# Kernel optimization log

Measured on AMD Instinct MI355X. Metric: run time of the kernel, lower is better.

## Reference

```python
import jax, jax.numpy as jnp
import numpy as np

S, B, IN = 8, 8192, 2      # obs seq_len, batch, input_size
E, H, OUT, PRED = 256, 1024, 2, 12  # embed, rnn_size, output_size, pred_len


def setup_inputs() -> dict:
    key = jax.random.key(0)
    ks = jax.random.split(key, 20)
    w = lambda k, shape, fan: (jax.random.normal(k, shape, jnp.float32) / np.sqrt(fan))
    return {
        "obs_traj": jax.random.normal(ks[0], (S, B, IN), jnp.float32),
        # input embedding Linear(IN -> E)
        "W_emb": w(ks[1], (E, IN), IN), "b_emb": jnp.zeros((E,), jnp.float32),
        # LSTM layer 0: input E -> H  (torch gate order i,f,g,o)
        "W_ih0": w(ks[2], (4 * H, E), E), "W_hh0": w(ks[3], (4 * H, H), H),
        "b_ih0": jnp.zeros((4 * H,), jnp.float32), "b_hh0": jnp.zeros((4 * H,), jnp.float32),
        # LSTM layer 1: input H -> H
        "W_ih1": w(ks[4], (4 * H, H), H), "W_hh1": w(ks[5], (4 * H, H), H),
        "b_ih1": jnp.zeros((4 * H,), jnp.float32), "b_hh1": jnp.zeros((4 * H,), jnp.float32),
        # output_seq MLP: H -> 32 -> 16 -> OUT
        "W1": w(ks[6], (32, H), H), "b1": jnp.zeros((32,), jnp.float32),
        "W2": w(ks[7], (16, 32), 32), "b2": jnp.zeros((16,), jnp.float32),
        "W3": w(ks[8], (OUT, 16), 16), "b3": jnp.zeros((OUT,), jnp.float32),
    }


def reference(obs_traj, W_emb, b_emb, W_ih0, W_hh0, b_ih0, b_hh0,
              W_ih1, W_hh1, b_ih1, b_hh1, W1, b1, W2, b2, W3, b3):
    # Dropout layers are identity in eval mode.
    def embed(x):
        return jax.nn.relu(x @ W_emb.T + b_emb)

    def cell(x, h, c, Wih, Whh, bih, bhh):
        g = x @ Wih.T + h @ Whh.T + (bih + bhh)          # [B, 4H]
        i, f, gg, o = jnp.split(g, 4, axis=-1)
        c = jax.nn.sigmoid(f) * c + jax.nn.sigmoid(i) * jnp.tanh(gg)
        h = jax.nn.sigmoid(o) * jnp.tanh(c)
        return h, c

    def lstm_step(hc, x):
        h0, c0, h1, c1 = hc
        h0, c0 = cell(x, h0, c0, W_ih0, W_hh0, b_ih0, b_hh0)
        h1, c1 = cell(h0, h1, c1, W_ih1, W_hh1, b_ih1, b_hh1)
        return (h0, c0, h1, c1), h1

    def mlp(h):
        h = jax.nn.relu(h @ W1.T + b1)
        h = jax.nn.relu(h @ W2.T + b2)
        return h @ W3.T + b3

    z = jnp.zeros((B, H), obs_traj.dtype)
    hc = (z, z, z, z)

    # --- encoding: run LSTM over the observed trajectory ---
    emb_obs = embed(obs_traj)                             # [S, B, E]
    hc, _ = jax.lax.scan(lambda c, x: lstm_step(c, x), hc, emb_obs)

    curr = obs_traj[-1]                                   # [B, IN]
    curr_emb = embed(curr)

    def dec_step(carry, _):
        hc, curr, curr_emb = carry
        hc, out = lstm_step(hc, curr_emb)                 # out: [B, H]
        nxt = curr + mlp(out)                             # displacement decode
        return (hc, nxt, embed(nxt)), nxt

    _, preds = jax.lax.scan(dec_step, (hc, curr, curr_emb), None, length=PRED)
    return preds                                          # [PRED, B, OUT]
```

## Files before the change

### kernel.cpp

```cpp
#include <hip/hip_runtime.h>
#include <hip/hip_bf16.h>
#include <stdint.h>

typedef __hip_bfloat16 bf16;
typedef __attribute__((ext_vector_type(8))) short bf16x8;
typedef __attribute__((ext_vector_type(4))) float f32x4;
typedef __attribute__((ext_vector_type(8))) unsigned short us8;

#define NB 8192
#define NE 256
#define NH 1024

__device__ __forceinline__ float bf2f(unsigned short u) {
  union { unsigned int i; float f; } x; x.i = ((unsigned int)u) << 16; return x.f;
}
__device__ __forceinline__ float sigm(float x) {
  return __builtin_amdgcn_rcpf(1.f + __expf(-x));
}
__device__ __forceinline__ float tanh_f(float x) {
  return 1.f - 2.f * __builtin_amdgcn_rcpf(1.f + __expf(2.f * x));
}

#define BAR() __builtin_amdgcn_s_barrier()
#define LGKM0() do { asm volatile("s_waitcnt lgkmcnt(0)" ::: "memory"); \
                     __builtin_amdgcn_sched_barrier(0); } while (0)
#define VMW(N) asm volatile("s_waitcnt vmcnt(" #N ")" ::: "memory")

#define MFMA32(MH)                                                            \
  do {                                                                        \
    __builtin_amdgcn_s_setprio(1);                                            \
    _Pragma("unroll") for (int i_ = 0; i_ < 4; ++i_)                          \
      _Pragma("unroll") for (int g_ = 0; g_ < 4; ++g_) {                      \
        acc[(MH)*4 + i_][g_] = __builtin_amdgcn_mfma_f32_16x16x32_bf16(       \
            af[i_], bv[g_], acc[(MH)*4 + i_][g_], 0, 0, 0);                   \
        acc[(MH)*4 + i_][g_] = __builtin_amdgcn_mfma_f32_16x16x32_bf16(       \
            af[4 + i_], bv[4 + g_], acc[(MH)*4 + i_][g_], 0, 0, 0);           \
      }                                                                       \
    __builtin_amdgcn_s_setprio(0);                                            \
  } while (0)

#define LDA8(BUF, MH)                                                         \
  do {                                                                        \
    const char* Ab_ = (const char*)&As[BUF][0][0];                            \
    _Pragma("unroll") for (int i_ = 0; i_ < 4; ++i_) {                        \
      int ro_ = (wr * 128 + (MH)*64 + i_ * 16 + l15) * 128;                   \
      af[i_]     = *(const bf16x8*)(Ab_ + ro_ + co0);                         \
      af[4 + i_] = *(const bf16x8*)(Ab_ + ro_ + co1);                         \
    }                                                                         \
  } while (0)

#define LDB8(BUF)                                                             \
  do {                                                                        \
    const char* Bb_ = (const char*)&Bs[BUF][0][0];                            \
    _Pragma("unroll") for (int g_ = 0; g_ < 4; ++g_) {                        \
      int ro_ = (g_ * 64 + nc * 16 + l15) * 128;                              \
      bv[g_]     = *(const bf16x8*)(Bb_ + ro_ + co0);                         \
      bv[4 + g_] = *(const bf16x8*)(Bb_ + ro_ + co1);                         \
    }                                                                         \
  } while (0)

__global__ __launch_bounds__(512, 2) void k_cell(
    const bf16* __restrict__ X, int ldx, int Kx,
    const bf16* __restrict__ Hin, int Kh,
    const bf16* __restrict__ Wih, const bf16* __restrict__ Whh,
    const float* __restrict__ bias, float* __restrict__ Cst,
    bf16* __restrict__ Hout, int czero)
{
  __shared__ bf16 As[2][256][64];
  __shared__ bf16 Bs[2][256][64];

  const int tid = threadIdx.x;
  const int l = tid & 63;
  const int l15 = l & 15;
  const int wv = tid >> 6;
  const int wr = wv >> 2;
  const int nc = wv & 3;

  const int bid = blockIdx.x;
  const int xcd = bid & 7, j = bid >> 3;
  const int m0 = (xcd * 4 + (j & 3)) * 256;
  const int hc0 = (j >> 2) * 64;

  const int NT = (Kx + Kh) >> 6;
  const int T = NT >> 1;

  const int rowid = tid >> 3;
  const int ch = (tid & 7) ^ (rowid & 7);
  const int wv8 = wv * 8;

  const int co0 = (((l >> 4) + 0) ^ (l & 7)) * 16;
  const int co1 = (((l >> 4) + 4) ^ (l & 7)) * 16;

  f32x4 acc[8][4];
  f32x4 zero4 = {0.f, 0.f, 0.f, 0.f};
#pragma unroll
  for (int i = 0; i < 8; ++i)
#pragma unroll
    for (int j2 = 0; j2 < 4; ++j2) acc[i][j2] = zero4;

  auto stage_a = [&](int buf, int half, int kt) {
    int kc = kt << 6;
    const bf16* src; size_t ld;
    if (kc < Kx) { src = X + kc; ld = (size_t)ldx; }
    else         { src = Hin + (kc - Kx); ld = NH; }
#pragma unroll
    for (int rnd = 0; rnd < 2; ++rnd) {
      int tr = rnd * 128 + half * 64;
      const bf16* gp = src + (size_t)(m0 + tr + rowid) * ld + ch * 8;
      __builtin_amdgcn_global_load_lds(
          (const __attribute__((address_space(1))) void*)gp,
          (__attribute__((address_space(3))) void*)&As[buf][tr + wv8][0],
          16, 0, 0);
    }
  };
  auto stage_b = [&](int buf, int half, int kt) {
    int kc = kt << 6;
    const bf16* src; size_t ld;
    if (kc < Kx) { src = Wih + kc; ld = (size_t)Kx; }
    else         { src = Whh + (kc - Kx); ld = NH; }
#pragma unroll
    for (int rnd = 0; rnd < 2; ++rnd) {
      int gate = rnd * 2 + half;
      const bf16* gp = src + (size_t)(gate * NH + hc0 + rowid) * ld + ch * 8;
      __builtin_amdgcn_global_load_lds(
          (const __attribute__((address_space(1))) void*)gp,
          (__attribute__((address_space(3))) void*)&Bs[buf][gate * 64 + wv8][0],
          16, 0, 0);
    }
  };

  stage_a(0, 0, 0);
  stage_a(0, 1, 0);
  stage_b(0, 0, 0);
  stage_b(0, 1, 0);
  stage_a(1, 0, 1);
  VMW(2);
  BAR();

  for (int t = 0; t < T; ++t) {
    const int kt1 = 2 * t + 1;
    const bool last = (t == T - 1);
    bf16x8 af[8], bv[8];

    stage_a(1, 1, kt1);
    stage_b(1, 0, kt1);
    stage_b(1, 1, kt1);
    LDB8(0); LDA8(0, 0);
    LGKM0();
    MFMA32(0);
    BAR();

    if (!last) stage_a(0, 0, kt1 + 1);
    LDA8(0, 1);
    LGKM0();
    MFMA32(1);
    if (last) { VMW(0); } else { VMW(2); }
    BAR();

    if (!last) {
      stage_a(0, 1, kt1 + 1);
      stage_b(0, 0, kt1 + 1);
      stage_b(0, 1, kt1 + 1);
    }
    LDB8(1); LDA8(1, 0);
    LGKM0();
    MFMA32(0);
    BAR();

    if (!last) stage_a(1, 0, kt1 + 2);
    LDA8(1, 1);
    LGKM0();
    MFMA32(1);
    if (!last) { VMW(2); }
    BAR();
  }

  const int ecol = hc0 + nc * 16 + l15;
  const float bi = bias[ecol];
  const float bff = bias[NH + ecol];
  const float bg = bias[2 * NH + ecol];
  const float bo = bias[3 * NH + ecol];
  const int r0 = m0 + wr * 128 + ((l >> 4) << 2);
#pragma unroll
  for (int m = 0; m < 8; ++m) {
#pragma unroll
    for (int r = 0; r < 4; ++r) {
      int row = r0 + m * 16 + r;
      size_t idx = (size_t)row * NH + ecol;
      float gi = sigm(acc[m][0][r] + bi);
      float gf = sigm(acc[m][1][r] + bff);
      float gg = tanh_f(acc[m][2][r] + bg);
      float go = sigm(acc[m][3][r] + bo);
      float cold = czero ? 0.f : Cst[idx];
      float cn = gf * cold + gi * gg;
      Cst[idx] = cn;
      Hout[idx] = __float2bfloat16(go * tanh_f(cn));
    }
  }
}

__global__ __launch_bounds__(256) void k_mlp(
    const bf16* __restrict__ h1, const bf16* __restrict__ W1b, const float* __restrict__ b1,
    const float* __restrict__ W2, const float* __restrict__ b2,
    const float* __restrict__ W3, const float* __restrict__ b3,
    const float* __restrict__ cin, float* __restrict__ cout,
    float* __restrict__ preds, const float* __restrict__ Wemb,
    const float* __restrict__ bemb, bf16* __restrict__ embout)
{
  const int l = threadIdx.x & 63;
  const int row = blockIdx.x * 4 + (threadIdx.x >> 6);

  const us8* hp = (const us8*)(h1 + (size_t)row * NH + l * 16);
  us8 hv0 = hp[0], hv1 = hp[1];
  float h[16];
#pragma unroll
  for (int j = 0; j < 8; ++j) { h[j] = bf2f(hv0[j]); h[8 + j] = bf2f(hv1[j]); }

  float y1[32];
#pragma unroll
  for (int j = 0; j < 32; ++j) {
    const us8* wp = (const us8*)(W1b + (size_t)j * NH + l * 16);
    us8 w0 = wp[0], w1 = wp[1];
    float d = 0.f;
#pragma unroll
    for (int k = 0; k < 8; ++k) {
      d = fmaf(h[k], bf2f(w0[k]), d);
      d = fmaf(h[8 + k], bf2f(w1[k]), d);
    }
#pragma unroll
    for (int off2 = 32; off2 > 0; off2 >>= 1) d += __shfl_xor(d, off2);
    y1[j] = fmaxf(d + b1[j], 0.f);
  }

  float y2[16];
#pragma unroll
  for (int m = 0; m < 16; ++m) {
    float s = b2[m];
#pragma unroll
    for (int j = 0; j < 32; ++j) s = fmaf(W2[m * 32 + j], y1[j], s);
    y2[m] = fmaxf(s, 0.f);
  }
  float o0 = b3[0], o1 = b3[1];
#pragma unroll
  for (int k = 0; k < 16; ++k) {
    o0 = fmaf(W3[k], y2[k], o0);
    o1 = fmaf(W3[16 + k], y2[k], o1);
  }
  float n0 = cin[row * 2] + o0;
  float n1 = cin[row * 2 + 1] + o1;
  if (l == 0) {
    preds[row * 2] = n0; preds[row * 2 + 1] = n1;
    cout[row * 2] = n0;  cout[row * 2 + 1] = n1;
  }
#pragma unroll
  for (int q = 0; q < 4; ++q) {
    int e = l + q * 64;
    float v = fmaf(n0, Wemb[e * 2], fmaf(n1, Wemb[e * 2 + 1], bemb[e]));
    embout[(size_t)row * NE + e] = __float2bfloat16(fmaxf(v, 0.f));
  }
}

__global__ void k_embed(const float* __restrict__ x, const float* __restrict__ W,
                        const float* __restrict__ b, bf16* __restrict__ out) {
  const int l = threadIdx.x & 63;
  const int row = (blockIdx.x * 256 + threadIdx.x) >> 6;
  float x0 = x[row * 2], x1 = x[row * 2 + 1];
#pragma unroll
  for (int q = 0; q < 4; ++q) {
    int e = l + q * 64;
    float v = fmaf(x0, W[e * 2], fmaf(x1, W[e * 2 + 1], b[e]));
    out[(size_t)row * NE + e] = __float2bfloat16(fmaxf(v, 0.f));
  }
}

__global__ void k_f2b(const float* __restrict__ in, bf16* __restrict__ out, int n) {
  int i = (blockIdx.x * 256 + threadIdx.x) * 4;
  if (i >= n) return;
  float4 v = *(const float4*)(in + i);
  out[i] = __float2bfloat16(v.x);
  out[i + 1] = __float2bfloat16(v.y);
  out[i + 2] = __float2bfloat16(v.z);
  out[i + 3] = __float2bfloat16(v.w);
}

__global__ void k_badd(const float* __restrict__ a, const float* __restrict__ b,
                       float* __restrict__ o, int n) {
  int i = blockIdx.x * 256 + threadIdx.x;
  if (i < n) o[i] = a[i] + b[i];
}

extern "C" void kernel_launch(void* const* d_in, const int* in_sizes, int n_in,
                              void* d_out, int out_size, void* d_ws, size_t ws_size,
                              hipStream_t stream) {
  const float* obs   = (const float*)d_in[0];
  const float* Wemb  = (const float*)d_in[1];
  const float* bemb  = (const float*)d_in[2];
  const float* Wih0f = (const float*)d_in[3];
  const float* Whh0f = (const float*)d_in[4];
  const float* bih0  = (const float*)d_in[5];
  const float* bhh0  = (const float*)d_in[6];
  const float* Wih1f = (const float*)d_in[7];
  const float* Whh1f = (const float*)d_in[8];
  const float* bih1  = (const float*)d_in[9];
  const float* bhh1  = (const float*)d_in[10];
  const float* W1f   = (const float*)d_in[11];
  const float* b1m   = (const float*)d_in[12];
  const float* W2    = (const float*)d_in[13];
  const float* b2    = (const float*)d_in[14];
  const float* W3    = (const float*)d_in[15];
  const float* b3    = (const float*)d_in[16];

  char* ws = (char*)d_ws;
  size_t off = 0;
  auto alloc = [&](size_t bytes) -> void* {
    void* p = ws + off;
    off += (bytes + 255) & ~(size_t)255;
    return p;
  };
  bf16* wih0 = (bf16*)alloc((size_t)4096 * 256 * 2);
  bf16* whh0 = (bf16*)alloc((size_t)4096 * 1024 * 2);
  bf16* wih1 = (bf16*)alloc((size_t)4096 * 1024 * 2);
  bf16* whh1 = (bf16*)alloc((size_t)4096 * 1024 * 2);
  bf16* w1b  = (bf16*)alloc((size_t)32 * 1024 * 2);
  float* b0c = (float*)alloc((size_t)4096 * 4);
  float* b1c = (float*)alloc((size_t)4096 * 4);
  bf16* emb  = (bf16*)alloc((size_t)8 * NB * NE * 2);
  bf16* h0a  = (bf16*)alloc((size_t)NB * NH * 2);
  bf16* h0b  = (bf16*)alloc((size_t)NB * NH * 2);
  bf16* h1a  = (bf16*)alloc((size_t)NB * NH * 2);
  bf16* h1b  = (bf16*)alloc((size_t)NB * NH * 2);
  float* c0  = (float*)alloc((size_t)NB * NH * 4);
  float* c1  = (float*)alloc((size_t)NB * NH * 4);
  float* curr = (float*)alloc((size_t)NB * 2 * 4);
  bf16* cemb = (bf16*)alloc((size_t)NB * NE * 2);

  k_f2b<<<1024, 256, 0, stream>>>(Wih0f, wih0, 4096 * 256);
  k_f2b<<<4096, 256, 0, stream>>>(Whh0f, whh0, 4096 * 1024);
  k_f2b<<<4096, 256, 0, stream>>>(Wih1f, wih1, 4096 * 1024);
  k_f2b<<<4096, 256, 0, stream>>>(Whh1f, whh1, 4096 * 1024);
  k_f2b<<<32, 256, 0, stream>>>(W1f, w1b, 32 * 1024);
  k_badd<<<16, 256, 0, stream>>>(bih0, bhh0, b0c, 4096);
  k_badd<<<16, 256, 0, stream>>>(bih1, bhh1, b1c, 4096);
  k_embed<<<(8 * NB) / 4, 256, 0, stream>>>(obs, Wemb, bemb, emb);

  bf16* h0buf[2] = {h0a, h0b};
  bf16* h1buf[2] = {h1a, h1b};
  float* preds = (float*)d_out;

  for (int t = 0; t < 20; ++t) {
    const bf16* xin;
    if (t < 8)       xin = emb + (size_t)t * NB * NE;
    else if (t == 8) xin = emb + (size_t)7 * NB * NE;
    else             xin = cemb;
    int cu = t & 1, pv = cu ^ 1;
    int kh = (t == 0) ? 0 : NH;
    k_cell<<<512, 512, 0, stream>>>(xin, NE, NE, h0buf[pv], kh,
                                    wih0, whh0, b0c, c0, h0buf[cu], t == 0);
    k_cell<<<512, 512, 0, stream>>>(h0buf[cu], NH, NH, h1buf[pv], kh,
                                    wih1, whh1, b1c, c1, h1buf[cu], t == 0);
    if (t >= 8) {
      int p = t - 8;
      const float* cin = (p == 0) ? (obs + (size_t)7 * NB * 2) : curr;
      k_mlp<<<NB / 4, 256, 0, stream>>>(h1buf[cu], w1b, b1m, W2, b2, W3, b3,
                                        cin, curr, preds + (size_t)p * NB * 2,
                                        Wemb, bemb, cemb);
    }
  }
}
```

Before: 5.458 ms.

## Restructure LSTM cell GEMM main loop into 4-stage K=32 LDS pipeline

Replaces the double-buffered K=64 tiles with four K=32 LDS buffers staged three tiles ahead. The main loop now interleaves the LDS fragment loads for the next tile between MFMA groups, using sched_group_barrier hints. It also uses precomputed global pointers and a new XOR swizzle. The goal is to hide global and LDS latency behind MFMA work, at the cost of more barriers per K and more complex tail handling.

```diff
diff --git a/kernel.cpp b/kernel.cpp
--- a/kernel.cpp
+++ b/kernel.cpp
@@ -26,37 +26,42 @@
                      __builtin_amdgcn_sched_barrier(0); } while (0)
 #define VMW(N) asm volatile("s_waitcnt vmcnt(" #N ")" ::: "memory")
 
-#define MFMA32(MH)                                                            \
+#define GLDS(G, S)                                                            \
+  __builtin_amdgcn_global_load_lds(                                           \
+      (const __attribute__((address_space(1))) void*)(G),                     \
+      (__attribute__((address_space(3))) void*)(S), 16, 0, 0)
+
+#define MM(M, G)                                                              \
+  acc[M][G] = __builtin_amdgcn_mfma_f32_16x16x32_bf16(af[M], bv[G], acc[M][G], 0, 0, 0)
+
+#define LDAF(N)                                                               \
+  do { _Pragma("unroll") for (int m_ = 0; m_ < 8; ++m_)                       \
+    af[m_] = *(const bf16x8*)(Aarena + base_a + ((N)*16384 + m_ * 1024));     \
+  } while (0)
+#define LDBV(N)                                                               \
+  do { _Pragma("unroll") for (int g_ = 0; g_ < 4; ++g_)                       \
+    bv[g_] = *(const bf16x8*)(Barena + base_b + ((N)*16384 + g_ * 4096));     \
+  } while (0)
+
+#define REGION(KT, CUR, NXT, STG, DOSTAGE, DOTRAIL, VKIND)                    \
   do {                                                                        \
+    if (DOSTAGE) stage(STG, (KT) + 3);                                        \
+    if ((VKIND) == 1) { VMW(4); }                                             \
+    if ((VKIND) == 2) { VMW(0); }                                             \
+    LGKM0();                                                                  \
     __builtin_amdgcn_s_setprio(1);                                            \
-    _Pragma("unroll") for (int i_ = 0; i_ < 4; ++i_)                          \
-      _Pragma("unroll") for (int g_ = 0; g_ < 4; ++g_) {                      \
-        acc[(MH)*4 + i_][g_] = __builtin_amdgcn_mfma_f32_16x16x32_bf16(       \
-            af[i_], bv[g_], acc[(MH)*4 + i_][g_], 0, 0, 0);                   \
-        acc[(MH)*4 + i_][g_] = __builtin_amdgcn_mfma_f32_16x16x32_bf16(       \
-            af[4 + i_], bv[4 + g_], acc[(MH)*4 + i_][g_], 0, 0, 0);           \
+    _Pragma("unroll")                                                         \
+    for (int m_ = 0; m_ < 8; ++m_) {                                          \
+      MM(m_, 0); MM(m_, 1); MM(m_, 2); MM(m_, 3);                             \
+      if (DOTRAIL) {                                                          \
+        af[m_] = *(const bf16x8*)(Aarena + base_a + ((NXT)*16384 + m_ * 1024)); \
+        __builtin_amdgcn_sched_group_barrier(0x8, 4, 0);                      \
+        __builtin_amdgcn_sched_group_barrier(0x100, 1, 0);                    \
       }                                                                       \
+    }                                                                         \
     __builtin_amdgcn_s_setprio(0);                                            \
-  } while (0)
-
-#define LDA8(BUF, MH)                                                         \
-  do {                                                                        \
-    const char* Ab_ = (const char*)&As[BUF][0][0];                            \
-    _Pragma("unroll") for (int i_ = 0; i_ < 4; ++i_) {                        \
-      int ro_ = (wr * 128 + (MH)*64 + i_ * 16 + l15) * 128;                   \
-      af[i_]     = *(const bf16x8*)(Ab_ + ro_ + co0);                         \
-      af[4 + i_] = *(const bf16x8*)(Ab_ + ro_ + co1);                         \
-    }                                                                         \
-  } while (0)
-
-#define LDB8(BUF)                                                             \
-  do {                                                                        \
-    const char* Bb_ = (const char*)&Bs[BUF][0][0];                            \
-    _Pragma("unroll") for (int g_ = 0; g_ < 4; ++g_) {                        \
-      int ro_ = (g_ * 64 + nc * 16 + l15) * 128;                              \
-      bv[g_]     = *(const bf16x8*)(Bb_ + ro_ + co0);                         \
-      bv[4 + g_] = *(const bf16x8*)(Bb_ + ro_ + co1);                         \
-    }                                                                         \
+    if (DOTRAIL) { LDBV(NXT); }                                               \
+    BAR();                                                                    \
   } while (0)
 
 __global__ __launch_bounds__(512, 2) void k_cell(
@@ -66,8 +71,8 @@
     const float* __restrict__ bias, float* __restrict__ Cst,
     bf16* __restrict__ Hout, int czero)
 {
-  __shared__ bf16 As[2][256][64];
-  __shared__ bf16 Bs[2][256][64];
+  __shared__ bf16 As[4][256][32];
+  __shared__ bf16 Bs[4][256][32];
 
   const int tid = threadIdx.x;
   const int l = tid & 63;
@@ -77,19 +82,28 @@
   const int nc = wv & 3;
 
   const int bid = blockIdx.x;
-  const int xcd = bid & 7, j = bid >> 3;
-  const int m0 = (xcd * 4 + (j & 3)) * 256;
-  const int hc0 = (j >> 2) * 64;
-
-  const int NT = (Kx + Kh) >> 6;
-  const int T = NT >> 1;
-
-  const int rowid = tid >> 3;
-  const int ch = (tid & 7) ^ (rowid & 7);
-  const int wv8 = wv * 8;
-
-  const int co0 = (((l >> 4) + 0) ^ (l & 7)) * 16;
-  const int co1 = (((l >> 4) + 4) ^ (l & 7)) * 16;
+  const int xcd = bid & 7, jj = bid >> 3;
+  const int m0 = (xcd * 4 + (jj & 3)) * 256;
+  const int hc0 = (jj >> 2) * 64;
+
+  const int NT32 = (Kx + Kh) >> 5;
+
+  const int ra0 = tid >> 2;
+  const int sch = (tid & 3) ^ ((tid >> 3) & 3);
+  const bf16* pAx = X + (size_t)(m0 + ra0) * ldx + sch * 8;
+  const bf16* pAh = Hin + (size_t)(m0 + ra0) * NH + sch * 8;
+  const size_t rAx2 = (size_t)128 * ldx, rAh2 = (size_t)128 * NH;
+  const int grow0 = (ra0 >> 6) * NH + hc0 + (ra0 & 63);
+  const bf16* pBx = Wih + (size_t)grow0 * Kx + sch * 8;
+  const bf16* pBh = Whh + (size_t)grow0 * NH + sch * 8;
+  const size_t rBx2 = (size_t)2 * NH * Kx, rBh2 = (size_t)2 * NH * NH;
+
+  char* Aarena = (char*)&As[0][0][0];
+  char* Barena = (char*)&Bs[0][0][0];
+
+  const int chp = (l >> 4) ^ ((l15 >> 1) & 3);
+  const int base_a = (wr * 128 + l15) * 64 + chp * 16;
+  const int base_b = (nc * 16 + l15) * 64 + chp * 16;
 
   f32x4 acc[8][4];
   f32x4 zero4 = {0.f, 0.f, 0.f, 0.f};
@@ -98,82 +112,43 @@
 #pragma unroll
     for (int j2 = 0; j2 < 4; ++j2) acc[i][j2] = zero4;
 
-  auto stage_a = [&](int buf, int half, int kt) {
-    int kc = kt << 6;
-    const bf16* src; size_t ld;
-    if (kc < Kx) { src = X + kc; ld = (size_t)ldx; }
-    else         { src = Hin + (kc - Kx); ld = NH; }
-#pragma unroll
-    for (int rnd = 0; rnd < 2; ++rnd) {
-      int tr = rnd * 128 + half * 64;
-      const bf16* gp = src + (size_t)(m0 + tr + rowid) * ld + ch * 8;
-      __builtin_amdgcn_global_load_lds(
-          (const __attribute__((address_space(1))) void*)gp,
-          (__attribute__((address_space(3))) void*)&As[buf][tr + wv8][0],
-          16, 0, 0);
+  auto stage = [&](int buf, int kt) {
+    int kc = kt << 5;
+    char* da = Aarena + buf * 16384 + tid * 16;
+    char* db = Barena + buf * 16384 + tid * 16;
+    if (kc < Kx) {
+      const bf16* a0 = pAx + kc;
+      GLDS(a0, da); GLDS(a0 + rAx2, da + 8192);
+      const bf16* b0 = pBx + kc;
+      GLDS(b0, db); GLDS(b0 + rBx2, db + 8192);
+    } else {
+      const bf16* a0 = pAh + (kc - Kx);
+      GLDS(a0, da); GLDS(a0 + rAh2, da + 8192);
+      const bf16* b0 = pBh + (kc - Kx);
+      GLDS(b0, db); GLDS(b0 + rBh2, db + 8192);
     }
   };
-  auto stage_b = [&](int buf, int half, int kt) {
-    int kc = kt << 6;
-    const bf16* src; size_t ld;
-    if (kc < Kx) { src = Wih + kc; ld = (size_t)Kx; }
-    else         { src = Whh + (kc - Kx); ld = NH; }
-#pragma unroll
-    for (int rnd = 0; rnd < 2; ++rnd) {
-      int gate = rnd * 2 + half;
-      const bf16* gp = src + (size_t)(gate * NH + hc0 + rowid) * ld + ch * 8;
-      __builtin_amdgcn_global_load_lds(
-          (const __attribute__((address_space(1))) void*)gp,
-          (__attribute__((address_space(3))) void*)&Bs[buf][gate * 64 + wv8][0],
-          16, 0, 0);
-    }
-  };
-
-  stage_a(0, 0, 0);
-  stage_a(0, 1, 0);
-  stage_b(0, 0, 0);
-  stage_b(0, 1, 0);
-  stage_a(1, 0, 1);
-  VMW(2);
+
+  bf16x8 af[8], bv[4];
+
+  stage(0, 0);
+  stage(1, 1);
+  stage(2, 2);
+  VMW(4);
   BAR();
-
-  for (int t = 0; t < T; ++t) {
-    const int kt1 = 2 * t + 1;
-    const bool last = (t == T - 1);
-    bf16x8 af[8], bv[8];
-
-    stage_a(1, 1, kt1);
-    stage_b(1, 0, kt1);
-    stage_b(1, 1, kt1);
-    LDB8(0); LDA8(0, 0);
-    LGKM0();
-    MFMA32(0);
-    BAR();
-
-    if (!last) stage_a(0, 0, kt1 + 1);
-    LDA8(0, 1);
-    LGKM0();
-    MFMA32(1);
-    if (last) { VMW(0); } else { VMW(2); }
-    BAR();
-
-    if (!last) {
-      stage_a(0, 1, kt1 + 1);
-      stage_b(0, 0, kt1 + 1);
-      stage_b(0, 1, kt1 + 1);
-    }
-    LDB8(1); LDA8(1, 0);
-    LGKM0();
-    MFMA32(0);
-    BAR();
-
-    if (!last) stage_a(1, 0, kt1 + 2);
-    LDA8(1, 1);
-    LGKM0();
-    MFMA32(1);
-    if (!last) { VMW(2); }
-    BAR();
-  }
+  LDAF(0); LDBV(0);
+
+  int kt = 0;
+  for (; kt < NT32 - 4; kt += 4) {
+    REGION(kt + 0, 0, 1, 3, 1, 1, 1);
+    REGION(kt + 1, 1, 2, 0, 1, 1, 1);
+    REGION(kt + 2, 2, 3, 1, 1, 1, 1);
+    REGION(kt + 3, 3, 0, 2, 1, 1, 1);
+  }
+  REGION(kt + 0, 0, 1, 3, 1, 1, 1);
+  REGION(kt + 1, 1, 2, 0, 0, 1, 2);
+  REGION(kt + 2, 2, 3, 0, 0, 1, 0);
+  REGION(kt + 3, 3, 0, 0, 0, 0, 0);
 
   const int ecol = hc0 + nc * 16 + l15;
   const float bi = bias[ecol];
```

New measurement: 7.548 ms. +38.3%, slower.

## Co-launch layer-1 step t with layer-0 step t+1 and reorder LDS waits

Applied to the files above, without the earlier changes.

During encoding, layer-1 at step t and layer-0 at step t+1 are independent, so both run as halves of one 1024-block launch of a parameterised cell kernel. This cuts launch count and gives more concurrent blocks to overlap the two GEMMs. The inner loop also issues LDS fragment reads before the global-to-LDS prefetch and defers the lgkmcnt wait until after the MFMAs, adding a barrier per stage. Added barriers and larger grids could cause wave quantization instead of overlap.

```diff
diff --git a/kernel.cpp b/kernel.cpp
--- a/kernel.cpp
+++ b/kernel.cpp
@@ -22,9 +22,14 @@
 }
 
 #define BAR() __builtin_amdgcn_s_barrier()
-#define LGKM0() do { asm volatile("s_waitcnt lgkmcnt(0)" ::: "memory"); \
-                     __builtin_amdgcn_sched_barrier(0); } while (0)
+#define FENCE() asm volatile("" ::: "memory")
+#define LGKME() asm volatile("s_waitcnt lgkmcnt(0)" ::: "memory")
 #define VMW(N) asm volatile("s_waitcnt vmcnt(" #N ")" ::: "memory")
+
+#define GLDS(G, S)                                                            \
+  __builtin_amdgcn_global_load_lds(                                           \
+      (const __attribute__((address_space(1))) void*)(G),                     \
+      (__attribute__((address_space(3))) void*)(S), 16, 0, 0)
 
 #define MFMA32(MH)                                                            \
   do {                                                                        \
@@ -59,15 +64,20 @@
     }                                                                         \
   } while (0)
 
-__global__ __launch_bounds__(512, 2) void k_cell(
-    const bf16* __restrict__ X, int ldx, int Kx,
-    const bf16* __restrict__ Hin, int Kh,
-    const bf16* __restrict__ Wih, const bf16* __restrict__ Whh,
-    const float* __restrict__ bias, float* __restrict__ Cst,
-    bf16* __restrict__ Hout, int czero)
+struct CellP {
+  const bf16* X; const bf16* Hin;
+  const bf16* Wih; const bf16* Whh;
+  const float* bias; float* Cst; bf16* Hout;
+  int ldx, Kx, Kh, czero;
+};
+
+__global__ __launch_bounds__(512, 2) void k_cell(CellP PA, CellP PB, int nA)
 {
   __shared__ bf16 As[2][256][64];
   __shared__ bf16 Bs[2][256][64];
+
+  const CellP p = (blockIdx.x < (unsigned)nA) ? PA : PB;
+  const int bid = (blockIdx.x < (unsigned)nA) ? blockIdx.x : (blockIdx.x - nA);
 
   const int tid = threadIdx.x;
   const int l = tid & 63;
@@ -76,12 +86,11 @@
   const int wr = wv >> 2;
   const int nc = wv & 3;
 
-  const int bid = blockIdx.x;
   const int xcd = bid & 7, j = bid >> 3;
   const int m0 = (xcd * 4 + (j & 3)) * 256;
   const int hc0 = (j >> 2) * 64;
 
-  const int NT = (Kx + Kh) >> 6;
+  const int NT = (p.Kx + p.Kh) >> 6;
   const int T = NT >> 1;
 
   const int rowid = tid >> 3;
@@ -101,31 +110,25 @@
   auto stage_a = [&](int buf, int half, int kt) {
     int kc = kt << 6;
     const bf16* src; size_t ld;
-    if (kc < Kx) { src = X + kc; ld = (size_t)ldx; }
-    else         { src = Hin + (kc - Kx); ld = NH; }
+    if (kc < p.Kx) { src = p.X + kc; ld = (size_t)p.ldx; }
+    else           { src = p.Hin + (kc - p.Kx); ld = NH; }
 #pragma unroll
     for (int rnd = 0; rnd < 2; ++rnd) {
       int tr = rnd * 128 + half * 64;
       const bf16* gp = src + (size_t)(m0 + tr + rowid) * ld + ch * 8;
-      __builtin_amdgcn_global_load_lds(
-          (const __attribute__((address_space(1))) void*)gp,
-          (__attribute__((address_space(3))) void*)&As[buf][tr + wv8][0],
-          16, 0, 0);
+      GLDS(gp, &As[buf][tr + wv8][0]);
     }
   };
   auto stage_b = [&](int buf, int half, int kt) {
     int kc = kt << 6;
     const bf16* src; size_t ld;
-    if (kc < Kx) { src = Wih + kc; ld = (size_t)Kx; }
-    else         { src = Whh + (kc - Kx); ld = NH; }
+    if (kc < p.Kx) { src = p.Wih + kc; ld = (size_t)p.Kx; }
+    else           { src = p.Whh + (kc - p.Kx); ld = NH; }
 #pragma unroll
     for (int rnd = 0; rnd < 2; ++rnd) {
       int gate = rnd * 2 + half;
       const bf16* gp = src + (size_t)(gate * NH + hc0 + rowid) * ld + ch * 8;
-      __builtin_amdgcn_global_load_lds(
-          (const __attribute__((address_space(1))) void*)gp,
-          (__attribute__((address_space(3))) void*)&Bs[buf][gate * 64 + wv8][0],
-          16, 0, 0);
+      GLDS(gp, &Bs[buf][gate * 64 + wv8][0]);
     }
   };
 
@@ -142,44 +145,48 @@
     const bool last = (t == T - 1);
     bf16x8 af[8], bv[8];
 
+    LDB8(0); LDA8(0, 0);
     stage_a(1, 1, kt1);
     stage_b(1, 0, kt1);
     stage_b(1, 1, kt1);
-    LDB8(0); LDA8(0, 0);
-    LGKM0();
+    FENCE(); BAR();
     MFMA32(0);
+    LGKME();
     BAR();
 
+    LDA8(0, 1);
     if (!last) stage_a(0, 0, kt1 + 1);
-    LDA8(0, 1);
-    LGKM0();
+    FENCE(); BAR();
     MFMA32(1);
+    LGKME();
     if (last) { VMW(0); } else { VMW(2); }
     BAR();
 
+    LDB8(1); LDA8(1, 0);
     if (!last) {
       stage_a(0, 1, kt1 + 1);
       stage_b(0, 0, kt1 + 1);
       stage_b(0, 1, kt1 + 1);
     }
-    LDB8(1); LDA8(1, 0);
-    LGKM0();
+    FENCE(); BAR();
     MFMA32(0);
+    LGKME();
     BAR();
 
+    LDA8(1, 1);
     if (!last) stage_a(1, 0, kt1 + 2);
-    LDA8(1, 1);
-    LGKM0();
+    FENCE(); BAR();
     MFMA32(1);
+    LGKME();
     if (!last) { VMW(2); }
     BAR();
   }
 
   const int ecol = hc0 + nc * 16 + l15;
-  const float bi = bias[ecol];
-  const float bff = bias[NH + ecol];
-  const float bg = bias[2 * NH + ecol];
-  const float bo = bias[3 * NH + ecol];
+  const float bi = p.bias[ecol];
+  const float bff = p.bias[NH + ecol];
+  const float bg = p.bias[2 * NH + ecol];
+  const float bo = p.bias[3 * NH + ecol];
   const int r0 = m0 + wr * 128 + ((l >> 4) << 2);
 #pragma unroll
   for (int m = 0; m < 8; ++m) {
@@ -191,10 +198,10 @@
       float gf = sigm(acc[m][1][r] + bff);
       float gg = tanh_f(acc[m][2][r] + bg);
       float go = sigm(acc[m][3][r] + bo);
-      float cold = czero ? 0.f : Cst[idx];
+      float cold = p.czero ? 0.f : p.Cst[idx];
       float cn = gf * cold + gi * gg;
-      Cst[idx] = cn;
-      Hout[idx] = __float2bfloat16(go * tanh_f(cn));
+      p.Cst[idx] = cn;
+      p.Hout[idx] = __float2bfloat16(go * tanh_f(cn));
     }
   }
 }
@@ -347,23 +354,45 @@
   bf16* h1buf[2] = {h1a, h1b};
   float* preds = (float*)d_out;
 
-  for (int t = 0; t < 20; ++t) {
-    const bf16* xin;
-    if (t < 8)       xin = emb + (size_t)t * NB * NE;
-    else if (t == 8) xin = emb + (size_t)7 * NB * NE;
-    else             xin = cemb;
+  auto mk = [&](const bf16* X, int ldx, int Kx, const bf16* Hin, int Kh,
+                const bf16* Wih, const bf16* Whh, const float* bb, float* C,
+                bf16* Ho, int cz) {
+    CellP q;
+    q.X = X; q.Hin = Hin; q.Wih = Wih; q.Whh = Whh;
+    q.bias = bb; q.Cst = C; q.Hout = Ho;
+    q.ldx = ldx; q.Kx = Kx; q.Kh = Kh; q.czero = cz;
+    return q;
+  };
+
+  {
+    CellP p0 = mk(emb, NE, NE, h0buf[1], 0, wih0, whh0, b0c, c0, h0buf[0], 1);
+    k_cell<<<512, 512, 0, stream>>>(p0, p0, 512);
+  }
+  for (int t = 0; t < 8; ++t) {
     int cu = t & 1, pv = cu ^ 1;
-    int kh = (t == 0) ? 0 : NH;
-    k_cell<<<512, 512, 0, stream>>>(xin, NE, NE, h0buf[pv], kh,
-                                    wih0, whh0, b0c, c0, h0buf[cu], t == 0);
-    k_cell<<<512, 512, 0, stream>>>(h0buf[cu], NH, NH, h1buf[pv], kh,
-                                    wih1, whh1, b1c, c1, h1buf[cu], t == 0);
-    if (t >= 8) {
-      int p = t - 8;
-      const float* cin = (p == 0) ? (obs + (size_t)7 * NB * 2) : curr;
-      k_mlp<<<NB / 4, 256, 0, stream>>>(h1buf[cu], w1b, b1m, W2, b2, W3, b3,
-                                        cin, curr, preds + (size_t)p * NB * 2,
-                                        Wemb, bemb, cemb);
-    }
-  }
-}
+    int kh1 = (t == 0) ? 0 : NH;
+    CellP pl1 = mk(h0buf[cu], NH, NH, h1buf[pv], kh1,
+                   wih1, whh1, b1c, c1, h1buf[cu], t == 0);
+    const bf16* xnext = (t + 1 < 8) ? emb + (size_t)(t + 1) * NB * NE
+                                    : emb + (size_t)7 * NB * NE;
+    CellP pl0 = mk(xnext, NE, NE, h0buf[cu], NH,
+                   wih0, whh0, b0c, c0, h0buf[pv], 0);
+    k_cell<<<1024, 512, 0, stream>>>(pl1, pl0, 512);
+  }
+  for (int t = 8; t < 20; ++t) {
+    int cu = t & 1, pv = cu ^ 1;
+    if (t > 8) {
+      CellP pl0 = mk(cemb, NE, NE, h0buf[pv], NH,
+                     wih0, whh0, b0c, c0, h0buf[cu], 0);
+      k_cell<<<512, 512, 0, stream>>>(pl0, pl0, 512);
+    }
+    CellP pl1 = mk(h0buf[cu], NH, NH, h1buf[pv], NH,
+                   wih1, whh1, b1c, c1, h1buf[cu], 0);
+    k_cell<<<512, 512, 0, stream>>>(pl1, pl1, 512);
+    int pI = t - 8;
+    const float* cin = (pI == 0) ? (obs + (size_t)7 * NB * 2) : curr;
+    k_mlp<<<NB / 4, 256, 0, stream>>>(h1buf[cu], w1b, b1m, W2, b2, W3, b3,
+                                      cin, curr, preds + (size_t)pI * NB * 2,
+                                      Wemb, bemb, cemb);
+  }
+}
```

Result: faster. 4.994 ms (-8.5%).
